# Kernel tuning notes

Measured on AMD Instinct MI355X. Metric: run time of the kernel, lower is better.

Reference implementation:

```python
import jax, jax.numpy as jnp
import numpy as np

HIDDEN = 3072
N_HEADS = 16
Q_LORA = 1536
KV_LORA = 512
NOPE = 128
ROPE = 64
QK_HD = NOPE + ROPE  # 192
V_HD = 128
B, S = 2, 1024


def rms_norm(x, w, eps=1e-6):
    xf = x.astype(jnp.float32)
    var = jnp.mean(xf * xf, axis=-1, keepdims=True)
    return w * (xf * jax.lax.rsqrt(var + eps)).astype(x.dtype)


def apply_rope(x):
    # x: (b, s, h, d) with d even; interleaved pair rotation as in the source
    b, s, h, d = x.shape
    pos = jnp.arange(s, dtype=jnp.float32)
    inv_freq = 1.0 / (10000.0 ** (jnp.arange(0, d, 2, dtype=jnp.float32) / d))
    ang = pos[:, None] * inv_freq[None, :]          # (s, d/2)
    sin = jnp.sin(ang)[None, :, None, :]            # (1, s, 1, d/2)
    cos = jnp.cos(ang)[None, :, None, :]
    xr = x.reshape(b, s, h, d // 2, 2)
    x1, x2 = xr[..., 0], xr[..., 1]
    r1 = x1 * cos - x2 * sin
    r2 = x1 * sin + x2 * cos
    return jnp.stack([r1, r2], axis=-1).reshape(b, s, h, d)


def setup_inputs() -> dict:
    key = jax.random.key(0)
    ks = jax.random.split(key, 16)
    sc = 0.02
    inp = {
        "hidden_states": jax.random.normal(ks[0], (B, S, HIDDEN), jnp.float32),
        # causal additive mask (s, t): 0 on/below diagonal, -1e9 above
        "mask": jnp.where(jnp.tril(jnp.ones((S, S), bool)), 0.0, -1e9).astype(jnp.float32),
        "wq_a_w": jax.random.normal(ks[1], (Q_LORA, HIDDEN), jnp.float32) * sc,
        "wq_a_b": jnp.zeros((Q_LORA,), jnp.float32),
        "q_norm_w": jnp.ones((Q_LORA,), jnp.float32),
        "wq_b_w": jax.random.normal(ks[2], (HIDDEN, Q_LORA), jnp.float32) * sc,
        "wq_b_b": jnp.zeros((HIDDEN,), jnp.float32),
        "wkv_a_w": jax.random.normal(ks[3], (KV_LORA + ROPE, HIDDEN), jnp.float32) * sc,
        "wkv_a_b": jnp.zeros((KV_LORA + ROPE,), jnp.float32),
        "kv_norm_w": jnp.ones((KV_LORA,), jnp.float32),
        "wkv_b_w": jax.random.normal(ks[4], (N_HEADS * (NOPE + V_HD), KV_LORA), jnp.float32) * sc,
        "wkv_b_b": jnp.zeros((N_HEADS * (NOPE + V_HD),), jnp.float32),
        "wo_w": jax.random.normal(ks[5], (HIDDEN, N_HEADS * V_HD), jnp.float32) * sc,
        "wo_b": jnp.zeros((HIDDEN,), jnp.float32),
    }
    return inp


def reference(hidden_states, mask, wq_a_w, wq_a_b, q_norm_w, wq_b_w, wq_b_b,
              wkv_a_w, wkv_a_b, kv_norm_w, wkv_b_w, wkv_b_b, wo_w, wo_b):
    b, s, _ = hidden_states.shape
    scale = QK_HD ** (-0.5)

    # low-rank Q projection
    q_lat = hidden_states @ wq_a_w.T + wq_a_b                  # (b,s,q_lora)
    q = rms_norm(q_lat, q_norm_w) @ wq_b_w.T + wq_b_b          # (b,s,hidden)
    q = q.reshape(b, s, N_HEADS, QK_HD)
    q_nope, q_rope = q[..., :NOPE], q[..., NOPE:]
    q_rope = apply_rope(q_rope)
    q = jnp.concatenate([q_nope, q_rope], axis=-1)             # (b,s,h,192)

    # low-rank KV projection with decoupled rope key
    kv = hidden_states @ wkv_a_w.T + wkv_a_b                   # (b,s,kv_lora+rope)
    kv_lat, k_rope = kv[..., :KV_LORA], kv[..., KV_LORA:]
    k_rope = apply_rope(k_rope[:, :, None, :])                 # (b,s,1,64)
    kv = rms_norm(kv_lat, kv_norm_w) @ wkv_b_w.T + wkv_b_b
    kv = kv.reshape(b, s, N_HEADS, NOPE + V_HD)
    k_nope, v = kv[..., :NOPE], kv[..., NOPE:]
    k = jnp.concatenate([k_nope, jnp.broadcast_to(k_rope, (b, s, N_HEADS, ROPE))], axis=-1)

    # naive full attention, fp32 softmax (as in source)
    scores = jnp.einsum('bshd,bthd->bsht', q, k) * scale       # (b,s,h,t)
    scores = scores + mask[None, :, None, :]
    p = jax.nn.softmax(scores.astype(jnp.float32), axis=-1)
    out = jnp.einsum('bsht,bthd->bshd', p, v)                  # (b,s,h,v_hd)
    out = out.reshape(b, s, N_HEADS * V_HD)
    return out @ wo_w.T + wo_b
```

## Files before the change

kernel.cpp:

```cpp
#include <hip/hip_runtime.h>
#include <stdint.h>
#include <stddef.h>

#define NHEADS 16
#define QLORA  1536
#define KVLORA 512
#define QKH    192
#define VH     128
#define BB     2
#define SS     1024
#define MROWS  (BB*SS)
#define HID    3072

typedef __attribute__((ext_vector_type(4))) float fx4;
typedef __attribute__((ext_vector_type(4))) short sx4;
typedef __attribute__((ext_vector_type(8))) short sx8;

__device__ __forceinline__ short f2bf(float f) {
  uint32_t u = __builtin_bit_cast(uint32_t, f);
  u = (u + 0x7fffu + ((u >> 16) & 1u)) >> 16;
  return (short)u;
}
__device__ __forceinline__ float bf2f(short s) {
  uint32_t u = ((uint32_t)(uint16_t)s) << 16;
  return __builtin_bit_cast(float, u);
}
__device__ __forceinline__ void gl_lds16(const void* g, void* l) {
  __builtin_amdgcn_global_load_lds((const __attribute__((address_space(1))) void*)g,
                                   (__attribute__((address_space(3))) void*)l, 16, 0, 0);
}
__device__ __forceinline__ sx8 ldfrag(const short* p) {
  sx4 lo = *(const sx4*)p;
  sx4 hi = *(const sx4*)(p + 16);
  sx8 r;
  r[0]=lo[0]; r[1]=lo[1]; r[2]=lo[2]; r[3]=lo[3];
  r[4]=hi[0]; r[5]=hi[1]; r[6]=hi[2]; r[7]=hi[3];
  return r;
}
__device__ __forceinline__ sx8 ldfrag_swz(const short* lds, int row, int rowShorts,
                                          int baseChunk, int g) {
  const int r7 = row & 7;
  const int gh = g >> 1, lo4 = (g & 1) * 4;
  int ch0 = baseChunk + gh;
  int ch1 = baseChunk + 2 + gh;
  ch0 = (ch0 & ~7) | ((ch0 & 7) ^ r7);
  ch1 = (ch1 & ~7) | ((ch1 & 7) ^ r7);
  const short* base = lds + row * rowShorts;
  sx4 a = *(const sx4*)(base + ch0 * 8 + lo4);
  sx4 b = *(const sx4*)(base + ch1 * 8 + lo4);
  sx8 r;
  r[0]=a[0]; r[1]=a[1]; r[2]=a[2]; r[3]=a[3];
  r[4]=b[0]; r[5]=b[1]; r[6]=b[2]; r[7]=b[3];
  return r;
}
__device__ __forceinline__ sx8 ldfrag_swz32(const short* lds, int row, int g) {
  const int f = (row >> 1) & 3;
  const int c0 = (g >> 1) ^ f;
  const int c1 = (2 + (g >> 1)) ^ f;
  const int lo4 = (g & 1) * 4;
  const short* base = lds + row * 32;
  sx4 a = *(const sx4*)(base + c0 * 8 + lo4);
  sx4 b = *(const sx4*)(base + c1 * 8 + lo4);
  sx8 r;
  r[0]=a[0]; r[1]=a[1]; r[2]=a[2]; r[3]=a[3];
  r[4]=b[0]; r[5]=b[1]; r[6]=b[2]; r[7]=b[3];
  return r;
}

struct CvtSeg { const float* src; short* dst; int n4; };
__global__ void k_cvt6(CvtSeg s0, CvtSeg s1, CvtSeg s2, CvtSeg s3, CvtSeg s4, CvtSeg s5) {
  const CvtSeg segs[6] = {s0, s1, s2, s3, s4, s5};
  const int stride = gridDim.x * blockDim.x;
  const int t0 = blockIdx.x * blockDim.x + threadIdx.x;
#pragma unroll
  for (int s = 0; s < 6; ++s) {
    const float* src = segs[s].src;
    short* dst = segs[s].dst;
    const int n4 = segs[s].n4;
    for (int i = t0; i < n4; i += stride) {
      fx4 v = *(const fx4*)(src + (size_t)i * 4);
      sx4 o;
      o[0] = f2bf(v[0]); o[1] = f2bf(v[1]); o[2] = f2bf(v[2]); o[3] = f2bf(v[3]);
      *(sx4*)(dst + (size_t)i * 4) = o;
    }
  }
}

__global__ void k_rope_tab(float* __restrict__ tab) {
  int i = blockIdx.x * blockDim.x + threadIdx.x;
  if (i >= SS * 32) return;
  int pos = i >> 5, fi = i & 31;
  float inv = powf(10000.0f, -(float)fi / 32.0f);
  float ang = (float)pos * inv;
  tab[i * 2]     = cosf(ang);
  tab[i * 2 + 1] = sinf(ang);
}

struct GemmProb {
  const short* A; const short* Bt; const float* bias; void* C;
  int N; int K;
};

template <int MFR, int SPLITK>
__global__ __launch_bounds__(256, 4)
void k_gemm2(GemmProb p0, GemmProb p1, int nblk0) {
  constexpr int TM = MFR * 32;
  constexpr int MT = 2048 / TM;
  int nwg = gridDim.x;
  int bid = (blockIdx.x % 8) * (nwg >> 3) + (blockIdx.x >> 3);
  const GemmProb p = (bid < nblk0) ? p0 : p1;
  int lb = (bid < nblk0) ? bid : bid - nblk0;
  const int N = p.N, K = p.K;
  const int NT = (N + 127) >> 7;
  const int tiles = MT * NT;
  const int tile = lb % tiles;
  const int pi = (SPLITK > 1) ? (lb / tiles) : 0;
  const int m0 = (tile % MT) * TM;
  const int n0 = (tile / MT) * 128;
  const int Kc = K / SPLITK;
  const int k0 = pi * Kc;

  __shared__ short As[2][TM * 32];
  __shared__ short Bs[2][128 * 32];
  const int tid  = threadIdx.x;
  const int lane = tid & 63;
  const int g    = lane >> 4;
  const int r16  = lane & 15;
  const int wave = tid >> 6;
  const int wm   = (wave >> 1) * (TM / 2);
  const int wn   = (wave & 1) * 64;

  fx4 acc[MFR][4] = {};

#define STAGE(bufi, kk)                                                        \
  do {                                                                         \
    _Pragma("unroll")                                                          \
    for (int i = 0; i < MFR / 2; ++i) {                                        \
      int cc = tid + 256 * i;                                                  \
      int row = cc >> 2;                                                       \
      int sc = ((cc & 3) ^ (row >> 1)) & 3;                                    \
      gl_lds16(p.A + (size_t)(m0 + row) * K + (kk) + sc * 8,                   \
               &As[bufi][cc * 8]);                                             \
    }                                                                          \
    _Pragma("unroll")                                                          \
    for (int i = 0; i < 2; ++i) {                                              \
      int cc = tid + 256 * i;                                                  \
      int row = cc >> 2;                                                       \
      int sc = ((cc & 3) ^ (row >> 1)) & 3;                                    \
      int bn = n0 + row; if (bn > N - 1) bn = N - 1;                           \
      gl_lds16(p.Bt + (size_t)bn * K + (kk) + sc * 8, &Bs[bufi][cc * 8]);      \
    }                                                                          \
  } while (0)

  const int nk = Kc >> 5;
  STAGE(0, k0);
  __syncthreads();

  int cur = 0;
  for (int t = 0; t < nk - 1; ++t) {
    STAGE(cur ^ 1, k0 + (t + 1) * 32);
    {
      sx8 af[MFR], bfv[4];
#pragma unroll
      for (int mi = 0; mi < MFR; ++mi)
        af[mi] = ldfrag_swz32(&As[cur][0], wm + mi * 16 + r16, g);
#pragma unroll
      for (int ni = 0; ni < 4; ++ni)
        bfv[ni] = ldfrag_swz32(&Bs[cur][0], wn + ni * 16 + r16, g);
#pragma unroll
      for (int mi = 0; mi < MFR; ++mi)
#pragma unroll
        for (int ni = 0; ni < 4; ++ni)
          acc[mi][ni] = __builtin_amdgcn_mfma_f32_16x16x32_bf16(af[mi], bfv[ni], acc[mi][ni], 0, 0, 0);
    }
    __syncthreads();
    cur ^= 1;
  }
  {
    sx8 af[MFR], bfv[4];
#pragma unroll
    for (int mi = 0; mi < MFR; ++mi)
      af[mi] = ldfrag_swz32(&As[cur][0], wm + mi * 16 + r16, g);
#pragma unroll
    for (int ni = 0; ni < 4; ++ni)
      bfv[ni] = ldfrag_swz32(&Bs[cur][0], wn + ni * 16 + r16, g);
#pragma unroll
    for (int mi = 0; mi < MFR; ++mi)
#pragma unroll
      for (int ni = 0; ni < 4; ++ni)
        acc[mi][ni] = __builtin_amdgcn_mfma_f32_16x16x32_bf16(af[mi], bfv[ni], acc[mi][ni], 0, 0, 0);
  }
#undef STAGE

  if (SPLITK > 1) {
    float* Cp = (float*)p.C + (size_t)pi * 2048 * N;
#pragma unroll
    for (int mi = 0; mi < MFR; ++mi) {
      int mbase = m0 + wm + mi * 16 + 4 * g;
#pragma unroll
      for (int ni = 0; ni < 4; ++ni) {
        int ncol = n0 + wn + ni * 16 + r16;
        if (ncol < N) {
#pragma unroll
          for (int r = 0; r < 4; ++r)
            Cp[(size_t)(mbase + r) * N + ncol] = acc[mi][ni][r];
        }
      }
    }
  } else {
#pragma unroll
    for (int mi = 0; mi < MFR; ++mi) {
      int mbase = m0 + wm + mi * 16 + 4 * g;
#pragma unroll
      for (int ni = 0; ni < 4; ++ni) {
        int ncol = n0 + wn + ni * 16 + r16;
        if (ncol < N) {
          float bv = p.bias[ncol];
#pragma unroll
          for (int r = 0; r < 4; ++r)
            ((short*)p.C)[(size_t)(mbase + r) * N + ncol] = f2bf(acc[mi][ni][r] + bv);
        }
      }
    }
  }
}

__global__ __launch_bounds__(256)
void k_prep(const float* __restrict__ qp, const float* __restrict__ q_bias,
            const float* __restrict__ q_norm_w, short* __restrict__ qn,
            const float* __restrict__ kvp, const float* __restrict__ kv_bias,
            const float* __restrict__ kv_norm_w, short* __restrict__ kvn,
            short* __restrict__ kr, const float* __restrict__ tab) {
  const int row = blockIdx.x;
  const int t = threadIdx.x;
  const size_t QS = (size_t)2048 * QLORA;
  const size_t KS = (size_t)2048 * 576;

  float x[8];
  float s1 = 0.f, s2 = 0.f;
  if (t < 192) {
    const float* a = qp + (size_t)row * QLORA + t * 8;
    fx4 u0 = *(const fx4*)(a),          u1 = *(const fx4*)(a + 4);
    fx4 v0 = *(const fx4*)(a + QS),     v1 = *(const fx4*)(a + QS + 4);
    fx4 w0 = *(const fx4*)(a + 2 * QS), w1 = *(const fx4*)(a + 2 * QS + 4);
#pragma unroll
    for (int j = 0; j < 4; ++j) {
      x[j]     = u0[j] + v0[j] + w0[j] + q_bias[t * 8 + j];
      x[4 + j] = u1[j] + v1[j] + w1[j] + q_bias[t * 8 + 4 + j];
    }
#pragma unroll
    for (int j = 0; j < 8; ++j) s1 += x[j] * x[j];
  } else {
    const int c = t - 192;
    const float* a = kvp + (size_t)row * 576 + c * 8;
    fx4 u0 = *(const fx4*)(a),          u1 = *(const fx4*)(a + 4);
    fx4 v0 = *(const fx4*)(a + KS),     v1 = *(const fx4*)(a + KS + 4);
    fx4 w0 = *(const fx4*)(a + 2 * KS), w1 = *(const fx4*)(a + 2 * KS + 4);
#pragma unroll
    for (int j = 0; j < 4; ++j) {
      x[j]     = u0[j] + v0[j] + w0[j] + kv_bias[c * 8 + j];
      x[4 + j] = u1[j] + v1[j] + w1[j] + kv_bias[c * 8 + 4 + j];
    }
#pragma unroll
    for (int j = 0; j < 8; ++j) s2 += x[j] * x[j];
  }
#pragma unroll
  for (int o = 32; o >= 1; o >>= 1) {
    s1 += __shfl_xor(s1, o, 64);
    s2 += __shfl_xor(s2, o, 64);
  }
  __shared__ float r1[4], r2[4];
  if ((t & 63) == 0) { r1[t >> 6] = s1; r2[t >> 6] = s2; }
  __syncthreads();
  float qss = r1[0] + r1[1] + r1[2] + r1[3];
  float kss = r2[0] + r2[1] + r2[2] + r2[3];
  float qrs = 1.0f / sqrtf(qss / (float)QLORA + 1e-6f);
  float krs = 1.0f / sqrtf(kss / (float)KVLORA + 1e-6f);

  if (t < 192) {
    sx8 o;
#pragma unroll
    for (int j = 0; j < 8; ++j) o[j] = f2bf(x[j] * qrs * q_norm_w[t * 8 + j]);
    *(sx8*)(qn + (size_t)row * QLORA + t * 8) = o;
  } else {
    int c = t - 192;
    sx8 o;
#pragma unroll
    for (int j = 0; j < 8; ++j) o[j] = f2bf(x[j] * krs * kv_norm_w[c * 8 + j]);
    *(sx8*)(kvn + (size_t)row * KVLORA + c * 8) = o;
  }
  if (t < 8) {
    const float* a = kvp + (size_t)row * 576 + 512 + t * 8;
    fx4 u0 = *(const fx4*)(a),          u1 = *(const fx4*)(a + 4);
    fx4 v0 = *(const fx4*)(a + KS),     v1 = *(const fx4*)(a + KS + 4);
    fx4 w0 = *(const fx4*)(a + 2 * KS), w1 = *(const fx4*)(a + 2 * KS + 4);
    float y[8];
#pragma unroll
    for (int j = 0; j < 4; ++j) {
      y[j]     = u0[j] + v0[j] + w0[j] + kv_bias[512 + t * 8 + j];
      y[4 + j] = u1[j] + v1[j] + w1[j] + kv_bias[512 + t * 8 + 4 + j];
    }
    int pos = row & (SS - 1);
    sx8 o;
#pragma unroll
    for (int k = 0; k < 4; ++k) {
      int i = t * 4 + k;
      float c = tab[(pos * 32 + i) * 2], s = tab[(pos * 32 + i) * 2 + 1];
      o[2 * k]     = f2bf(y[2 * k] * c - y[2 * k + 1] * s);
      o[2 * k + 1] = f2bf(y[2 * k] * s + y[2 * k + 1] * c);
    }
    *(sx8*)(kr + (size_t)row * 64 + t * 8) = o;
  }
}

__global__ __launch_bounds__(256)
void k_post(const short* __restrict__ kvb, short* __restrict__ vt,
            short* __restrict__ qb, const float* __restrict__ tab) {
  const int bid = blockIdx.x;
  const int tid = threadIdx.x;
  if (bid < 512) {
    const int bh = bid >> 4;
    const int t0 = (bid & 15) * 64;
    const int b = bh >> 4, h = bh & 15;
    __shared__ short sm[64 * 128];
#pragma unroll
    for (int i = 0; i < 4; ++i) {
      int c = tid + 256 * i;
      int tt = c >> 4, d0 = (c & 15) * 8;
      sx8 v = *(const sx8*)(kvb + ((size_t)(b * SS + t0 + tt)) * 4096 + h * 256 + 128 + d0);
      *(sx8*)(sm + tt * 128 + d0) = v;
    }
    __syncthreads();
#pragma unroll
    for (int i = 0; i < 4; ++i) {
      int c = tid + 256 * i;
      int d = c >> 3, tof = (c & 7) * 8;
      sx8 v;
#pragma unroll
      for (int j = 0; j < 8; ++j) v[j] = sm[(tof + j) * 128 + d];
      *(sx8*)(vt + ((size_t)bh * VH + d) * SS + t0 + tof) = v;
    }
  } else {
    int p = (bid - 512) * 256 + tid;
    int j = p & 7, h = (p >> 3) & 15, row = p >> 7;
    int pos = row & (SS - 1);
    size_t base = (((size_t)row * NHEADS + h) * QKH) + 128 + j * 8;
    sx8 x = *(const sx8*)(qb + base);
    sx8 o;
#pragma unroll
    for (int k = 0; k < 4; ++k) {
      int i = j * 4 + k;
      float c = tab[(pos * 32 + i) * 2], s = tab[(pos * 32 + i) * 2 + 1];
      float x1 = bf2f(x[2 * k]), x2 = bf2f(x[2 * k + 1]);
      o[2 * k]     = f2bf(x1 * c - x2 * s);
      o[2 * k + 1] = f2bf(x1 * s + x2 * c);
    }
    *(sx8*)(qb + base) = o;
  }
}

__global__ __launch_bounds__(256)
void k_osum(const float* __restrict__ p, const float* __restrict__ bias,
            float* __restrict__ out) {
  const size_t OS = (size_t)2048 * HID;
  int i = blockIdx.x * 256 + threadIdx.x;
  fx4 a = *(const fx4*)(p + (size_t)i * 4);
  fx4 b = *(const fx4*)(p + OS + (size_t)i * 4);
  int col = (i * 4) % HID;
  fx4 bv = *(const fx4*)(bias + col);
  fx4 o = a + b + bv;
  *(fx4*)(out + (size_t)i * 4) = o;
}

__global__ __launch_bounds__(256, 2)
void k_attn(const short* __restrict__ q, const short* __restrict__ kvb,
            const short* __restrict__ kr, const short* __restrict__ vt,
            short* __restrict__ ao) {
  const int bh = blockIdx.x;
  const int b = bh >> 4, h = bh & 15;
  const int qt0 = blockIdx.y * 64;
  const int tid = threadIdx.x;
  const int lane = tid & 63;
  const int wave = tid >> 6;
  const int g = lane >> 4, r16 = lane & 15;
  const int qg = qt0 + wave * 16 + r16;

  __shared__ short Ks[64 * QKH];
  __shared__ short Vs[VH * 64];

  sx8 qf[6];
  {
    const short* qr = q + (((size_t)(b * SS + qg)) * NHEADS + h) * QKH;
#pragma unroll
    for (int f = 0; f < 6; ++f) qf[f] = ldfrag(qr + f * 32 + 4 * g);
  }

  float mrun = -1e30f, lrun = 0.0f;
  fx4 oacc[8] = {};
  const float scale = 0.07216878364870323f;

  const int ntiles = qt0 / 64 + 1;
  for (int kt = 0; kt < ntiles; ++kt) {
    const int t0 = kt * 64;
#pragma unroll
    for (int i = 0; i < 6; ++i) {
      int cc = tid + 256 * i;
      int row = cc / 24, ch = cc % 24;
      int sc = (ch & 24) | ((ch & 7) ^ (row & 7));
      size_t grow = (size_t)(b * SS + t0 + row);
      const short* src = (sc < 16) ? kvb + grow * 4096 + h * 256 + sc * 8
                                   : kr + grow * 64 + (sc - 16) * 8;
      gl_lds16(src, &Ks[cc * 8]);
    }
#pragma unroll
    for (int i = 0; i < 4; ++i) {
      int cc = tid + 256 * i;
      int row = cc >> 3;
      int sc = (cc & 7) ^ (row & 7);
      gl_lds16(vt + ((size_t)bh * VH + row) * SS + t0 + sc * 8, &Vs[cc * 8]);
    }
    __syncthreads();

    const bool diag = (kt == ntiles - 1);
    float pv[16];
    float tmax = -1e30f;
#pragma unroll
    for (int th = 0; th < 4; ++th) {
      fx4 sacc = {};
#pragma unroll
      for (int f = 0; f < 6; ++f) {
        sx8 kf = ldfrag_swz(Ks, th * 16 + r16, QKH, f * 4, g);
        sacc = __builtin_amdgcn_mfma_f32_16x16x32_bf16(kf, qf[f], sacc, 0, 0, 0);
      }
#pragma unroll
      for (int r = 0; r < 4; ++r) {
        int t = t0 + th * 16 + 4 * g + r;
        float s = sacc[r] * scale;
        if (diag && t > qg) s = -1e30f;
        pv[th * 4 + r] = s;
        tmax = fmaxf(tmax, s);
      }
    }
    tmax = fmaxf(tmax, __shfl_xor(tmax, 16, 64));
    tmax = fmaxf(tmax, __shfl_xor(tmax, 32, 64));
    float mnew = fmaxf(mrun, tmax);
    float corr = __expf(mrun - mnew);
    float psum = 0.f;
#pragma unroll
    for (int j = 0; j < 16; ++j) { pv[j] = __expf(pv[j] - mnew); psum += pv[j]; }
    psum += __shfl_xor(psum, 16, 64);
    psum += __shfl_xor(psum, 32, 64);
    lrun = lrun * corr + psum;
    mrun = mnew;
#pragma unroll
    for (int f8 = 0; f8 < 8; ++f8) oacc[f8] *= corr;

    sx8 pf0, pf1;
#pragma unroll
    for (int j = 0; j < 8; ++j) { pf0[j] = f2bf(pv[j]); pf1[j] = f2bf(pv[8 + j]); }

#pragma unroll
    for (int f8 = 0; f8 < 8; ++f8) {
      sx8 v0 = ldfrag_swz(Vs, f8 * 16 + r16, 64, 0, g);
      sx8 v1 = ldfrag_swz(Vs, f8 * 16 + r16, 64, 4, g);
      oacc[f8] = __builtin_amdgcn_mfma_f32_16x16x32_bf16(v0, pf0, oacc[f8], 0, 0, 0);
      oacc[f8] = __builtin_amdgcn_mfma_f32_16x16x32_bf16(v1, pf1, oacc[f8], 0, 0, 0);
    }
    __syncthreads();
  }

  float inv = 1.0f / lrun;
#pragma unroll
  for (int f8 = 0; f8 < 8; ++f8)
#pragma unroll
    for (int r = 0; r < 4; ++r) {
      int d = f8 * 16 + 4 * g + r;
      ao[(((size_t)(b * SS + qg)) * NHEADS + h) * VH + d] = f2bf(oacc[f8][r] * inv);
    }
}

extern "C" void kernel_launch(void* const* d_in, const int* in_sizes, int n_in,
                              void* d_out, int out_size, void* d_ws, size_t ws_size,
                              hipStream_t stream) {
  const float* hs       = (const float*)d_in[0];
  const float* wq_a_w   = (const float*)d_in[2];
  const float* wq_a_b   = (const float*)d_in[3];
  const float* q_norm_w = (const float*)d_in[4];
  const float* wq_b_w   = (const float*)d_in[5];
  const float* wq_b_b   = (const float*)d_in[6];
  const float* wkv_a_w  = (const float*)d_in[7];
  const float* wkv_a_b  = (const float*)d_in[8];
  const float* kv_norm_w= (const float*)d_in[9];
  const float* wkv_b_w  = (const float*)d_in[10];
  const float* wkv_b_b  = (const float*)d_in[11];
  const float* wo_w     = (const float*)d_in[12];
  const float* wo_b     = (const float*)d_in[13];
  float* out = (float*)d_out;

  short* ws0 = (short*)d_ws;
  size_t off = 0;
  short* wqa_bf  = ws0 + off; off += (size_t)QLORA * HID;
  short* wqb_bf  = ws0 + off; off += (size_t)HID * QLORA;
  short* wkva_bf = ws0 + off; off += (size_t)576 * HID;
  short* wkvb_bf = ws0 + off; off += (size_t)4096 * KVLORA;
  short* wo_bf   = ws0 + off; off += (size_t)HID * 2048;
  short* h_bf    = ws0 + off; off += (size_t)MROWS * HID;
  short* qn      = ws0 + off; off += (size_t)MROWS * QLORA;
  short* kvn     = ws0 + off; off += (size_t)MROWS * KVLORA;
  short* kr      = ws0 + off; off += (size_t)MROWS * 64;
  short* qb      = ws0 + off; off += (size_t)MROWS * HID;
  short* kvb     = ws0 + off; off += (size_t)MROWS * 4096;
  short* vtb     = ws0 + off; off += (size_t)BB * NHEADS * VH * SS;
  short* ao      = ws0 + off; off += (size_t)MROWS * 2048;
  float* tab     = (float*)(ws0 + off + (off & 1));
  float* arena   = tab + SS * 64;
  float* qlatp   = arena;
  float* kvp     = arena + (size_t)3 * 2048 * QLORA;
  float* wop     = arena;

  {
    CvtSeg s0{wq_a_w,  wqa_bf,  (int)((size_t)QLORA * HID / 4)};
    CvtSeg s1{wq_b_w,  wqb_bf,  (int)((size_t)HID * QLORA / 4)};
    CvtSeg s2{wkv_a_w, wkva_bf, (int)((size_t)576 * HID / 4)};
    CvtSeg s3{wkv_b_w, wkvb_bf, (int)((size_t)4096 * KVLORA / 4)};
    CvtSeg s4{wo_w,    wo_bf,   (int)((size_t)HID * 2048 / 4)};
    CvtSeg s5{hs,      h_bf,    (int)((size_t)MROWS * HID / 4)};
    k_cvt6<<<2048, 256, 0, stream>>>(s0, s1, s2, s3, s4, s5);
  }
  k_rope_tab<<<(SS * 32 + 255) / 256, 256, 0, stream>>>(tab);

  {
    GemmProb pq{h_bf, wqa_bf,  nullptr, qlatp, QLORA, HID};
    GemmProb pk{h_bf, wkva_bf, nullptr, kvp,   576,   HID};
    int nb0 = 16 * (QLORA / 128) * 3;
    int nb1 = 16 * ((576 + 127) / 128) * 3;
    k_gemm2<4, 3><<<nb0 + nb1, 256, 0, stream>>>(pq, pk, nb0);
  }

  k_prep<<<MROWS, 256, 0, stream>>>(qlatp, wq_a_b, q_norm_w, qn,
                                    kvp, wkv_a_b, kv_norm_w, kvn, kr, tab);

  {
    GemmProb pq{qn,  wqb_bf,  wq_b_b,  qb,  HID,  QLORA};
    GemmProb pk{kvn, wkvb_bf, wkv_b_b, kvb, 4096, KVLORA};
    int nb0 = 16 * (HID / 128);
    int nb1 = 16 * (4096 / 128);
    k_gemm2<4, 1><<<nb0 + nb1, 256, 0, stream>>>(pq, pk, nb0);
  }

  k_post<<<512 + 1024, 256, 0, stream>>>(kvb, vtb, qb, tab);

  k_attn<<<dim3(BB * NHEADS, SS / 64), 256, 0, stream>>>(qb, kvb, kr, vtb, ao);

  {
    GemmProb po{ao, wo_bf, nullptr, wop, HID, 2048};
    int nb = 16 * (HID / 128) * 2;
    k_gemm2<4, 2><<<nb, 256, 0, stream>>>(po, po, nb);
  }
  k_osum<<<(MROWS * HID / 4) / 256, 256, 0, stream>>>(wop, wo_b, out);
}
```

Measured before the change: 253.1 us.

## Triple-buffer GEMM LDS staging with explicit vmcnt waits and single barrier

Turns the double-buffered GEMM mainloop into a three-stage pipeline. Loads are issued two K-steps ahead, each iteration waits with s_waitcnt vmcnt(4) and uses one barrier instead of two __syncthreads. This is meant to hide global-to-LDS latency and cut synchronisation per step. In exchange it uses more shared memory (occupancy hint lowered to 3 blocks per CU). It also depends on the async LDS load count matching the hardcoded vmcnt value.

```diff
diff --git a/kernel.cpp b/kernel.cpp
--- a/kernel.cpp
+++ b/kernel.cpp
@@ -102,8 +102,8 @@
 };
 
 template <int MFR, int SPLITK>
-__global__ __launch_bounds__(256, 4)
-void k_gemm2(GemmProb p0, GemmProb p1, int nblk0) {
+__global__ __launch_bounds__(256, 3)
+void k_gemm3(GemmProb p0, GemmProb p1, int nblk0) {
   constexpr int TM = MFR * 32;
   constexpr int MT = 2048 / TM;
   int nwg = gridDim.x;
@@ -120,8 +120,8 @@
   const int Kc = K / SPLITK;
   const int k0 = pi * Kc;
 
-  __shared__ short As[2][TM * 32];
-  __shared__ short Bs[2][128 * 32];
+  __shared__ short As[3][TM * 32];
+  __shared__ short Bs[3][128 * 32];
   const int tid  = threadIdx.x;
   const int lane = tid & 63;
   const int g    = lane >> 4;
@@ -154,41 +154,30 @@
 
   const int nk = Kc >> 5;
   STAGE(0, k0);
-  __syncthreads();
-
-  int cur = 0;
-  for (int t = 0; t < nk - 1; ++t) {
-    STAGE(cur ^ 1, k0 + (t + 1) * 32);
+  STAGE(1, k0 + 32);
+
+  int c0 = 0, c1 = 1, c2 = 2;
+  for (int t = 0; t < nk; ++t) {
+    if (t < nk - 1) asm volatile("s_waitcnt vmcnt(4)" ::: "memory");
+    else            asm volatile("s_waitcnt vmcnt(0)" ::: "memory");
+    __builtin_amdgcn_s_barrier();
+    __builtin_amdgcn_sched_barrier(0);
+    if (t + 2 < nk) STAGE(c2, k0 + (t + 2) * 32);
     {
       sx8 af[MFR], bfv[4];
 #pragma unroll
       for (int mi = 0; mi < MFR; ++mi)
-        af[mi] = ldfrag_swz32(&As[cur][0], wm + mi * 16 + r16, g);
+        af[mi] = ldfrag_swz32(&As[c0][0], wm + mi * 16 + r16, g);
 #pragma unroll
       for (int ni = 0; ni < 4; ++ni)
-        bfv[ni] = ldfrag_swz32(&Bs[cur][0], wn + ni * 16 + r16, g);
+        bfv[ni] = ldfrag_swz32(&Bs[c0][0], wn + ni * 16 + r16, g);
 #pragma unroll
       for (int mi = 0; mi < MFR; ++mi)
 #pragma unroll
         for (int ni = 0; ni < 4; ++ni)
           acc[mi][ni] = __builtin_amdgcn_mfma_f32_16x16x32_bf16(af[mi], bfv[ni], acc[mi][ni], 0, 0, 0);
     }
-    __syncthreads();
-    cur ^= 1;
-  }
-  {
-    sx8 af[MFR], bfv[4];
-#pragma unroll
-    for (int mi = 0; mi < MFR; ++mi)
-      af[mi] = ldfrag_swz32(&As[cur][0], wm + mi * 16 + r16, g);
-#pragma unroll
-    for (int ni = 0; ni < 4; ++ni)
-      bfv[ni] = ldfrag_swz32(&Bs[cur][0], wn + ni * 16 + r16, g);
-#pragma unroll
-    for (int mi = 0; mi < MFR; ++mi)
-#pragma unroll
-      for (int ni = 0; ni < 4; ++ni)
-        acc[mi][ni] = __builtin_amdgcn_mfma_f32_16x16x32_bf16(af[mi], bfv[ni], acc[mi][ni], 0, 0, 0);
+    int tmp = c0; c0 = c1; c1 = c2; c2 = tmp;
   }
 #undef STAGE
 
@@ -534,7 +523,7 @@
     GemmProb pk{h_bf, wkva_bf, nullptr, kvp,   576,   HID};
     int nb0 = 16 * (QLORA / 128) * 3;
     int nb1 = 16 * ((576 + 127) / 128) * 3;
-    k_gemm2<4, 3><<<nb0 + nb1, 256, 0, stream>>>(pq, pk, nb0);
+    k_gemm3<4, 3><<<nb0 + nb1, 256, 0, stream>>>(pq, pk, nb0);
   }
 
   k_prep<<<MROWS, 256, 0, stream>>>(qlatp, wq_a_b, q_norm_w, qn,
@@ -545,7 +534,7 @@
     GemmProb pk{kvn, wkvb_bf, wkv_b_b, kvb, 4096, KVLORA};
     int nb0 = 16 * (HID / 128);
     int nb1 = 16 * (4096 / 128);
-    k_gemm2<4, 1><<<nb0 + nb1, 256, 0, stream>>>(pq, pk, nb0);
+    k_gemm3<4, 1><<<nb0 + nb1, 256, 0, stream>>>(pq, pk, nb0);
   }
 
   k_post<<<512 + 1024, 256, 0, stream>>>(kvb, vtb, qb, tab);
@@ -555,7 +544,7 @@
   {
     GemmProb po{ao, wo_bf, nullptr, wop, HID, 2048};
     int nb = 16 * (HID / 128) * 2;
-    k_gemm2<4, 2><<<nb, 256, 0, stream>>>(po, po, nb);
+    k_gemm3<4, 2><<<nb, 256, 0, stream>>>(po, po, nb);
   }
   k_osum<<<(MROWS * HID / 4) / 256, 256, 0, stream>>>(wop, wo_b, out);
 }
```

Result: slower. 288.5 us (+14.0%).
